# Kernel optimization log

Hardware: AMD Instinct MI355X
Metric: run time of the kernel (lower is better)

## Reference

```python
import jax, jax.numpy as jnp
import numpy as np

LEAKY_SLOPE = 0.2  # tf.nn.leaky_relu default alpha
NEG_INF = -1e9


def setup_inputs() -> dict:
    key = jax.random.key(0)
    k1, k2, k3, k4 = jax.random.split(key, 4)
    B, N, F, D, H = 1, 4096, 128, 64, 4
    features = jax.random.normal(k1, (B, N, F), dtype=jnp.float32)
    adj = jax.random.randint(k2, (N, N), 0, 2, dtype=jnp.int32)  # 0/1 adjacency
    W = jax.random.normal(k3, (H, F, D), dtype=jnp.float32) * 0.1
    attn_k = jax.random.normal(k4, (H, 2 * D, 1), dtype=jnp.float32) * 0.1
    return {"adj": adj, "features": features, "W": W, "attn_k": attn_k}


def reference(adj, features, W, attn_k):
    H, _, D = W.shape
    adj_f = adj.astype(jnp.float32)[None]       # [1, N, N], broadcast over batch
    mask = adj_f != 0.0
    outs = []
    for i in range(H):  # fixed small head loop (heads are structurally distinct weights)
        h = features @ W[i]                      # [B, N, D]
        a_self = h @ attn_k[i, :D]               # [B, N, 1]
        a_neigh = h @ attn_k[i, D:]              # [B, N, 1]
        scores = a_self + jnp.swapaxes(a_neigh, 1, 2)  # [B, N, N] additive scores
        scores = jax.nn.leaky_relu(scores, LEAKY_SLOPE)
        scores = jnp.where(mask, scores, NEG_INF)
        attn = jax.nn.softmax(scores, axis=-1)   # [B, N, N]
        outs.append((attn * adj_f) @ h)          # [B, N, D]
    out = jnp.concatenate(outs, axis=-1) if H > 1 else outs[0]
    return jax.nn.relu(out)
```

## Files before the change

### kernel.cpp

```cpp
#include <hip/hip_runtime.h>
#include <math.h>

#define NN 4096
#define FF 128
#define DD 64
#define HH 4
#define NC 256

typedef _Float16 f16x8 __attribute__((ext_vector_type(8)));
typedef _Float16 f16x2 __attribute__((ext_vector_type(2)));
typedef float    f32x4 __attribute__((ext_vector_type(4)));

__global__ __launch_bounds__(256) void adjbits_kernel(
    const int* __restrict__ adj, unsigned int* __restrict__ adjw)
{
    const int w = blockIdx.x * 256 + threadIdx.x;
    const int4* __restrict__ p = (const int4*)(adj + (size_t)w * 32);
    unsigned int m = 0;
    #pragma unroll
    for (int i = 0; i < 8; ++i) {
        const int4 v = p[i];
        m |= (v.x != 0 ? 1u : 0u) << (i * 4);
        m |= (v.y != 0 ? 2u : 0u) << (i * 4);
        m |= (v.z != 0 ? 4u : 0u) << (i * 4);
        m |= (v.w != 0 ? 8u : 0u) << (i * 4);
    }
    adjw[w] = m;
}

__global__ __launch_bounds__(256) void prep_kernel(
    const float* __restrict__ feats, const float* __restrict__ W,
    const float* __restrict__ ak, _Float16* __restrict__ Bpack,
    _Float16* __restrict__ Es, _Float16* __restrict__ Fs,
    _Float16* __restrict__ En, _Float16* __restrict__ Fn)
{
    __shared__ float Wt[64 * 132];
    __shared__ float ft[32 * 128];
    __shared__ float hlds[32 * 65];
    const int t  = threadIdx.x;
    const int h  = blockIdx.y;
    const int n0 = blockIdx.x * 32;

    {
        const float* Wh = W + h * (FF * DD);
        #pragma unroll
        for (int j = 0; j < 8; ++j) {
            int idx = j * 256 + t;
            int f   = idx >> 4;
            int d4  = idx & 15;
            float4 v = ((const float4*)Wh)[idx];
            Wt[(d4 * 4 + 0) * 132 + f] = v.x;
            Wt[(d4 * 4 + 1) * 132 + f] = v.y;
            Wt[(d4 * 4 + 2) * 132 + f] = v.z;
            Wt[(d4 * 4 + 3) * 132 + f] = v.w;
        }
        #pragma unroll
        for (int j = 0; j < 4; ++j) {
            int idx = j * 256 + t;
            int r = idx >> 5, f4 = idx & 31;
            ((float4*)ft)[r * 32 + f4] = ((const float4*)feats)[(size_t)(n0 + r) * 32 + f4];
        }
    }
    __syncthreads();

    const int d   = t & 63;
    const int wid = t >> 6;
    float acc[8];
    #pragma unroll
    for (int j = 0; j < 8; ++j) acc[j] = 0.f;

    for (int f4 = 0; f4 < 32; ++f4) {
        const float4 w4 = *(const float4*)&Wt[d * 132 + f4 * 4];
        #pragma unroll
        for (int j = 0; j < 8; ++j) {
            const int r = wid + 4 * j;
            const float4 fv = *(const float4*)&ft[r * 128 + f4 * 4];
            acc[j] += fv.x * w4.x + fv.y * w4.y + fv.z * w4.z + fv.w * w4.w;
        }
    }

    const float aks = ak[h * 128 + d];
    const float akn = ak[h * 128 + 64 + d];
    #pragma unroll
    for (int j = 0; j < 8; ++j) {
        const int r = wid + 4 * j;
        const float hv = acc[j];
        hlds[r * 65 + d] = hv;
        float v1 = hv * aks;
        float v2 = hv * akn;
        #pragma unroll
        for (int m = 32; m >= 1; m >>= 1) {
            v1 += __shfl_xor(v1, m, 64);
            v2 += __shfl_xor(v2, m, 64);
        }
        if (d == 0) {
            Es[h * NN + n0 + r] = (_Float16)__expf(v1);
            Fs[h * NN + n0 + r] = (_Float16)__expf(0.2f * v1);
            En[h * NN + n0 + r] = (_Float16)__expf(v2);
            Fn[h * NN + n0 + r] = (_Float16)__expf(0.2f * v2);
        }
    }
    __syncthreads();

    const int cb = t >> 6;
    const int l  = t & 63;
    const int lr = l & 15;
    const int kg = l >> 4;
    f16x8 v;
    #pragma unroll
    for (int j = 0; j < 8; ++j)
        v[j] = (_Float16)hlds[(kg * 8 + j) * 65 + cb * 16 + lr];
    *(f16x8*)(Bpack + ((size_t)(h * 128 + blockIdx.x)) * 2048 + (cb * 64 + l) * 8) = v;
}

__global__ __launch_bounds__(256, 4) void attn_kernel(
    const unsigned int* __restrict__ adjw, const _Float16* __restrict__ Bpack,
    const _Float16* __restrict__ Es, const _Float16* __restrict__ Fs,
    const _Float16* __restrict__ En, const _Float16* __restrict__ Fn,
    float* __restrict__ pacc, float* __restrict__ pden, int ksplit)
{
    __shared__ _Float16 Blds[2][2048];

    const int t  = threadIdx.x;
    const int w  = t >> 6;
    const int l  = t & 63;
    const int lr = l & 15;
    const int kg = l >> 4;
    const int h  = blockIdx.y;
    const int s  = blockIdx.z;
    const int n0 = blockIdx.x * 128 + w * 32;

    const int mstart = s * ksplit;
    const int nchunk = ksplit >> 5;
    const int ncq    = nchunk >> 2;
    const int coff   = blockIdx.x & (ncq - 1);
    const int wb     = mstart >> 5;

#define PC(c) (((((c) >> 2) + coff) & (ncq - 1)) * 4 + ((c) & 3))

    const _Float16 es0 = Es[h * NN + n0 + lr],      fs0 = Fs[h * NN + n0 + lr];
    const _Float16 es1 = Es[h * NN + n0 + 16 + lr], fs1 = Fs[h * NN + n0 + 16 + lr];
    const f16x2 es20 = {es0, es0}, fs20 = {fs0, fs0};
    const f16x2 es21 = {es1, es1}, fs21 = {fs1, fs1};

    const _Float16* __restrict__ EnB = En + (size_t)h * NN;
    const _Float16* __restrict__ FnB = Fn + (size_t)h * NN;
    const int row0 = n0 + lr, row1 = n0 + 16 + lr;

    const _Float16* __restrict__ bp =
        Bpack + ((size_t)(h * 128) + wb) * 2048 + t * 8;

    f32x4 acc[2][4] = {};
    f32x4 dacc[2]   = {};
    f16x8 ones;
    #pragma unroll
    for (int j = 0; j < 8; ++j) ones[j] = (_Float16)1.0f;

    union U8 { f16x8 v; unsigned int u[4]; };

    uint4 sreg = *(const uint4*)(bp + (size_t)PC(0) * 2048);
    *(uint4*)&Blds[0][t * 8] = sreg;
    sreg = *(const uint4*)(bp + (size_t)PC(1) * 2048);
    uint4 enqc = *(const uint4*)(EnB + mstart + PC(0) * 32 + kg * 8);
    uint4 fnqc = *(const uint4*)(FnB + mstart + PC(0) * 32 + kg * 8);
    __syncthreads();

    for (int cq = 0; cq < ncq; ++cq) {
        const int cqp = (cq + coff) & (ncq - 1);
        const uint4 mk0 = *(const uint4*)&adjw[(size_t)row0 * 128 + wb + cqp * 4];
        const uint4 mk1 = *(const uint4*)&adjw[(size_t)row1 * 128 + wb + cqp * 4];

        #pragma unroll
        for (int ci = 0; ci < 4; ++ci) {
            const int c = cq * 4 + ci;

            uint4 nreg;
            {
                const int cn = (c + 2 < nchunk) ? c + 2 : c;
                nreg = *(const uint4*)(bp + (size_t)PC(cn) * 2048);
            }
            if (c + 1 < nchunk)
                *(uint4*)&Blds[(c + 1) & 1][t * 8] = sreg;
            uint4 enq_n, fnq_n;
            {
                const int cn = (c + 1 < nchunk) ? c + 1 : c;
                enq_n = *(const uint4*)(EnB + mstart + PC(cn) * 32 + kg * 8);
                fnq_n = *(const uint4*)(FnB + mstart + PC(cn) * 32 + kg * 8);
            }

            const unsigned int b0 =
                (ci == 0 ? mk0.x : ci == 1 ? mk0.y : ci == 2 ? mk0.z : mk0.w) >> (kg * 8);
            const unsigned int b1 =
                (ci == 0 ? mk1.x : ci == 1 ? mk1.y : ci == 2 ? mk1.z : mk1.w) >> (kg * 8);
            U8 A0, A1;
            #pragma unroll
            for (int p = 0; p < 4; ++p) {
                const unsigned int eu = p == 0 ? enqc.x : p == 1 ? enqc.y : p == 2 ? enqc.z : enqc.w;
                const unsigned int fu = p == 0 ? fnqc.x : p == 1 ? fnqc.y : p == 2 ? fnqc.z : fnqc.w;
                const f16x2 en2 = __builtin_bit_cast(f16x2, eu);
                const f16x2 fn2 = __builtin_bit_cast(f16x2, fu);
                const f16x2 v0 = __builtin_elementwise_max(es20 * en2, fs20 * fn2);
                const f16x2 v1 = __builtin_elementwise_max(es21 * en2, fs21 * fn2);
                const unsigned int mm0 = (((b0 >> (2 * p)) & 1u) ? 0x0000FFFFu : 0u)
                                       | (((b0 >> (2 * p + 1)) & 1u) ? 0xFFFF0000u : 0u);
                const unsigned int mm1 = (((b1 >> (2 * p)) & 1u) ? 0x0000FFFFu : 0u)
                                       | (((b1 >> (2 * p + 1)) & 1u) ? 0xFFFF0000u : 0u);
                A0.u[p] = __builtin_bit_cast(unsigned int, v0) & mm0;
                A1.u[p] = __builtin_bit_cast(unsigned int, v1) & mm1;
            }

            __builtin_amdgcn_s_setprio(1);
            #pragma unroll
            for (int cb = 0; cb < 4; ++cb) {
                const f16x8 Bf = *(const f16x8*)&Blds[c & 1][(cb * 64 + l) * 8];
                acc[0][cb] = __builtin_amdgcn_mfma_f32_16x16x32_f16(A0.v, Bf, acc[0][cb], 0, 0, 0);
                acc[1][cb] = __builtin_amdgcn_mfma_f32_16x16x32_f16(A1.v, Bf, acc[1][cb], 0, 0, 0);
            }
            dacc[0] = __builtin_amdgcn_mfma_f32_16x16x32_f16(A0.v, ones, dacc[0], 0, 0, 0);
            dacc[1] = __builtin_amdgcn_mfma_f32_16x16x32_f16(A1.v, ones, dacc[1], 0, 0, 0);
            __builtin_amdgcn_s_setprio(0);

            __syncthreads();
            sreg = nreg;
            enqc = enq_n;
            fnqc = fnq_n;
        }
    }
#undef PC

    #pragma unroll
    for (int rb = 0; rb < 2; ++rb) {
        #pragma unroll
        for (int r = 0; r < 4; ++r) {
            const int row = n0 + rb * 16 + kg * 4 + r;
            #pragma unroll
            for (int cb = 0; cb < 4; ++cb)
                pacc[((size_t)(s * NN + row)) * NC + h * 64 + cb * 16 + lr] = acc[rb][cb][r];
            if (lr == 0)
                pden[(s * NN + row) * 4 + h] = dacc[rb][r];
        }
    }
}

__global__ __launch_bounds__(256) void finalize_kernel(
    const float* __restrict__ pacc, const float* __restrict__ pden,
    float* __restrict__ out, int nsplit)
{
    const int t = threadIdx.x;
    const int n = blockIdx.x * 4 + (t >> 6);
    const int q = t & 63;
    const int h = q >> 4;

    f32x4 a = {0.f, 0.f, 0.f, 0.f};
    float d = 0.f;
    for (int s = 0; s < nsplit; ++s) {
        a += *(const f32x4*)&pacc[((size_t)(s * NN + n)) * NC + q * 4];
        d += pden[(s * NN + n) * 4 + h];
    }
    f32x4 o;
    const float inv = (d > 0.f) ? 1.0f / d : 0.f;
    #pragma unroll
    for (int i = 0; i < 4; ++i) {
        const float v = a[i] * inv;
        o[i] = v > 0.f ? v : 0.f;
    }
    *(f32x4*)&out[(size_t)n * NC + q * 4] = o;
}

extern "C" void kernel_launch(void* const* d_in, const int* in_sizes, int n_in,
                              void* d_out, int out_size, void* d_ws, size_t ws_size,
                              hipStream_t stream)
{
    const int*   adj   = (const int*)d_in[0];
    const float* feats = (const float*)d_in[1];
    const float* W     = (const float*)d_in[2];
    const float* ak    = (const float*)d_in[3];
    float*       out   = (float*)d_out;

    char* ws = (char*)d_ws;
    unsigned int* adjw  = (unsigned int*)ws;
    _Float16*     Bpack = (_Float16*)(ws + (2ull << 20));
    _Float16*     Es    = (_Float16*)(ws + (4ull << 20));
    _Float16*     Fs    = (_Float16*)(ws + (4ull << 20) + (1 << 16));
    _Float16*     En    = (_Float16*)(ws + (4ull << 20) + (2 << 16));
    _Float16*     Fn    = (_Float16*)(ws + (4ull << 20) + (3 << 16));
    float*        pden  = (float*)(ws + (4ull << 20) + (4 << 16));
    float*        pacc  = (float*)(ws + (5ull << 20));

    int nsplit = 8;
    while (nsplit > 1 && ws_size < (5ull << 20) + (size_t)nsplit * (4ull << 20))
        nsplit >>= 1;
    const int ksplit = NN / nsplit;

    adjbits_kernel<<<2048, 256, 0, stream>>>(adj, adjw);
    prep_kernel<<<dim3(128, 4), 256, 0, stream>>>(feats, W, ak, Bpack, Es, Fs, En, Fn);
    attn_kernel<<<dim3(32, 4, nsplit), 256, 0, stream>>>(adjw, Bpack, Es, Fs, En, Fn,
                                                         pacc, pden, ksplit);
    finalize_kernel<<<1024, 256, 0, stream>>>(pacc, pden, out, nsplit);
}
```

Measured before the change: 55.81 us.

## Pack adjacency bits with wave ballots and use fp16 dot2 in projection

The adjacency bitpacking kernel now has each wave read contiguous int4 rows and build masks with __ballot, which gives fully coalesced loads of the 64MB adjacency matrix. The result is a new interleaved bit layout that the attention kernel decodes with different shift logic. The prep projection now stores W and features in LDS as fp16 and accumulates with fdot2 instead of fp32 FMAs. This lowers projection precision to fp16 inputs, which risks extra error in h and in the attention logits.

```diff
diff --git a/kernel.cpp b/kernel.cpp
--- a/kernel.cpp
+++ b/kernel.cpp
@@ -8,24 +8,31 @@
 #define NC 256
 
 typedef _Float16 f16x8 __attribute__((ext_vector_type(8)));
+typedef _Float16 f16x4 __attribute__((ext_vector_type(4)));
 typedef _Float16 f16x2 __attribute__((ext_vector_type(2)));
 typedef float    f32x4 __attribute__((ext_vector_type(4)));
 
 __global__ __launch_bounds__(256) void adjbits_kernel(
-    const int* __restrict__ adj, unsigned int* __restrict__ adjw)
-{
-    const int w = blockIdx.x * 256 + threadIdx.x;
-    const int4* __restrict__ p = (const int4*)(adj + (size_t)w * 32);
-    unsigned int m = 0;
+    const int* __restrict__ adj, uint4* __restrict__ adjp)
+{
+    const int wid  = blockIdx.x * 4 + (threadIdx.x >> 6);
+    const int lane = threadIdx.x & 63;
+    const int4* __restrict__ base = (const int4*)adj;
     #pragma unroll
     for (int i = 0; i < 8; ++i) {
-        const int4 v = p[i];
-        m |= (v.x != 0 ? 1u : 0u) << (i * 4);
-        m |= (v.y != 0 ? 2u : 0u) << (i * 4);
-        m |= (v.z != 0 ? 4u : 0u) << (i * 4);
-        m |= (v.w != 0 ? 8u : 0u) << (i * 4);
-    }
-    adjw[w] = m;
+        const int g = wid * 8 + i;
+        const int4 v = base[(size_t)g * 64 + lane];
+        unsigned long long b0 = __ballot(v.x != 0);
+        unsigned long long b1 = __ballot(v.y != 0);
+        unsigned long long b2 = __ballot(v.z != 0);
+        unsigned long long b3 = __ballot(v.w != 0);
+        if (lane == 0) {
+            adjp[g * 2] = (uint4){(unsigned)b0, (unsigned)b1,
+                                  (unsigned)b2, (unsigned)b3};
+            adjp[g * 2 + 1] = (uint4){(unsigned)(b0 >> 32), (unsigned)(b1 >> 32),
+                                      (unsigned)(b2 >> 32), (unsigned)(b3 >> 32)};
+        }
+    }
 }
 
 __global__ __launch_bounds__(256) void prep_kernel(
@@ -34,9 +41,9 @@
     _Float16* __restrict__ Es, _Float16* __restrict__ Fs,
     _Float16* __restrict__ En, _Float16* __restrict__ Fn)
 {
-    __shared__ float Wt[64 * 132];
-    __shared__ float ft[32 * 128];
-    __shared__ float hlds[32 * 65];
+    __shared__ _Float16 Wth[64 * 136];
+    __shared__ _Float16 fth[32 * 128];
+    __shared__ float    hlds[32 * 65];
     const int t  = threadIdx.x;
     const int h  = blockIdx.y;
     const int n0 = blockIdx.x * 32;
@@ -49,16 +56,18 @@
             int f   = idx >> 4;
             int d4  = idx & 15;
             float4 v = ((const float4*)Wh)[idx];
-            Wt[(d4 * 4 + 0) * 132 + f] = v.x;
-            Wt[(d4 * 4 + 1) * 132 + f] = v.y;
-            Wt[(d4 * 4 + 2) * 132 + f] = v.z;
-            Wt[(d4 * 4 + 3) * 132 + f] = v.w;
+            Wth[(d4 * 4 + 0) * 136 + f] = (_Float16)v.x;
+            Wth[(d4 * 4 + 1) * 136 + f] = (_Float16)v.y;
+            Wth[(d4 * 4 + 2) * 136 + f] = (_Float16)v.z;
+            Wth[(d4 * 4 + 3) * 136 + f] = (_Float16)v.w;
         }
         #pragma unroll
         for (int j = 0; j < 4; ++j) {
             int idx = j * 256 + t;
             int r = idx >> 5, f4 = idx & 31;
-            ((float4*)ft)[r * 32 + f4] = ((const float4*)feats)[(size_t)(n0 + r) * 32 + f4];
+            float4 v = ((const float4*)feats)[(size_t)(n0 + r) * 32 + f4];
+            f16x4 hv = {(_Float16)v.x, (_Float16)v.y, (_Float16)v.z, (_Float16)v.w};
+            *(f16x4*)&fth[r * 128 + f4 * 4] = hv;
         }
     }
     __syncthreads();
@@ -69,13 +78,20 @@
     #pragma unroll
     for (int j = 0; j < 8; ++j) acc[j] = 0.f;
 
-    for (int f4 = 0; f4 < 32; ++f4) {
-        const float4 w4 = *(const float4*)&Wt[d * 132 + f4 * 4];
+    for (int f8 = 0; f8 < 16; ++f8) {
+        const f16x8 w8 = *(const f16x8*)&Wth[d * 136 + f8 * 8];
+        const f16x2 w0 = __builtin_shufflevector(w8, w8, 0, 1);
+        const f16x2 w1 = __builtin_shufflevector(w8, w8, 2, 3);
+        const f16x2 w2 = __builtin_shufflevector(w8, w8, 4, 5);
+        const f16x2 w3 = __builtin_shufflevector(w8, w8, 6, 7);
         #pragma unroll
         for (int j = 0; j < 8; ++j) {
             const int r = wid + 4 * j;
-            const float4 fv = *(const float4*)&ft[r * 128 + f4 * 4];
-            acc[j] += fv.x * w4.x + fv.y * w4.y + fv.z * w4.z + fv.w * w4.w;
+            const f16x8 fv = *(const f16x8*)&fth[r * 128 + f8 * 8];
+            acc[j] = __builtin_amdgcn_fdot2(w0, __builtin_shufflevector(fv, fv, 0, 1), acc[j], false);
+            acc[j] = __builtin_amdgcn_fdot2(w1, __builtin_shufflevector(fv, fv, 2, 3), acc[j], false);
+            acc[j] = __builtin_amdgcn_fdot2(w2, __builtin_shufflevector(fv, fv, 4, 5), acc[j], false);
+            acc[j] = __builtin_amdgcn_fdot2(w3, __builtin_shufflevector(fv, fv, 6, 7), acc[j], false);
         }
     }
 
@@ -114,7 +130,7 @@
 }
 
 __global__ __launch_bounds__(256, 4) void attn_kernel(
-    const unsigned int* __restrict__ adjw, const _Float16* __restrict__ Bpack,
+    const uint4* __restrict__ adjp, const _Float16* __restrict__ Bpack,
     const _Float16* __restrict__ Es, const _Float16* __restrict__ Fs,
     const _Float16* __restrict__ En, const _Float16* __restrict__ Fn,
     float* __restrict__ pacc, float* __restrict__ pden, int ksplit)
@@ -134,7 +150,7 @@
     const int nchunk = ksplit >> 5;
     const int ncq    = nchunk >> 2;
     const int coff   = blockIdx.x & (ncq - 1);
-    const int wb     = mstart >> 5;
+    const int wqb    = mstart >> 7;
 
 #define PC(c) (((((c) >> 2) + coff) & (ncq - 1)) * 4 + ((c) & 3))
 
@@ -145,10 +161,11 @@
 
     const _Float16* __restrict__ EnB = En + (size_t)h * NN;
     const _Float16* __restrict__ FnB = Fn + (size_t)h * NN;
-    const int row0 = n0 + lr, row1 = n0 + 16 + lr;
+    const uint4* __restrict__ adjpR0 = adjp + (size_t)(n0 + lr) * 32;
+    const uint4* __restrict__ adjpR1 = adjp + (size_t)(n0 + 16 + lr) * 32;
 
     const _Float16* __restrict__ bp =
-        Bpack + ((size_t)(h * 128) + wb) * 2048 + t * 8;
+        Bpack + ((size_t)(h * 128) + (mstart >> 5)) * 2048 + t * 8;
 
     f32x4 acc[2][4] = {};
     f32x4 dacc[2]   = {};
@@ -167,8 +184,8 @@
 
     for (int cq = 0; cq < ncq; ++cq) {
         const int cqp = (cq + coff) & (ncq - 1);
-        const uint4 mk0 = *(const uint4*)&adjw[(size_t)row0 * 128 + wb + cqp * 4];
-        const uint4 mk1 = *(const uint4*)&adjw[(size_t)row1 * 128 + wb + cqp * 4];
+        const uint4 mk0 = adjpR0[wqb + cqp];
+        const uint4 mk1 = adjpR1[wqb + cqp];
 
         #pragma unroll
         for (int ci = 0; ci < 4; ++ci) {
@@ -188,10 +205,21 @@
                 fnq_n = *(const uint4*)(FnB + mstart + PC(cn) * 32 + kg * 8);
             }
 
-            const unsigned int b0 =
-                (ci == 0 ? mk0.x : ci == 1 ? mk0.y : ci == 2 ? mk0.z : mk0.w) >> (kg * 8);
-            const unsigned int b1 =
-                (ci == 0 ? mk1.x : ci == 1 ? mk1.y : ci == 2 ? mk1.z : mk1.w) >> (kg * 8);
+            const int q = ci * 8 + kg * 2;
+            const unsigned int t0 = mk0.x >> q, t1 = mk0.y >> q;
+            const unsigned int t2 = mk0.z >> q, t3 = mk0.w >> q;
+            const unsigned int u0 = mk1.x >> q, u1 = mk1.y >> q;
+            const unsigned int u2 = mk1.z >> q, u3 = mk1.w >> q;
+            unsigned int mmA[4], mmB[4];
+            mmA[0] = ((t0 & 1u) ? 0x0000FFFFu : 0u) | ((t1 & 1u) ? 0xFFFF0000u : 0u);
+            mmA[1] = ((t2 & 1u) ? 0x0000FFFFu : 0u) | ((t3 & 1u) ? 0xFFFF0000u : 0u);
+            mmA[2] = (((t0 >> 1) & 1u) ? 0x0000FFFFu : 0u) | (((t1 >> 1) & 1u) ? 0xFFFF0000u : 0u);
+            mmA[3] = (((t2 >> 1) & 1u) ? 0x0000FFFFu : 0u) | (((t3 >> 1) & 1u) ? 0xFFFF0000u : 0u);
+            mmB[0] = ((u0 & 1u) ? 0x0000FFFFu : 0u) | ((u1 & 1u) ? 0xFFFF0000u : 0u);
+            mmB[1] = ((u2 & 1u) ? 0x0000FFFFu : 0u) | ((u3 & 1u) ? 0xFFFF0000u : 0u);
+            mmB[2] = (((u0 >> 1) & 1u) ? 0x0000FFFFu : 0u) | (((u1 >> 1) & 1u) ? 0xFFFF0000u : 0u);
+            mmB[3] = (((u2 >> 1) & 1u) ? 0x0000FFFFu : 0u) | (((u3 >> 1) & 1u) ? 0xFFFF0000u : 0u);
+
             U8 A0, A1;
             #pragma unroll
             for (int p = 0; p < 4; ++p) {
@@ -201,12 +229,8 @@
                 const f16x2 fn2 = __builtin_bit_cast(f16x2, fu);
                 const f16x2 v0 = __builtin_elementwise_max(es20 * en2, fs20 * fn2);
                 const f16x2 v1 = __builtin_elementwise_max(es21 * en2, fs21 * fn2);
-                const unsigned int mm0 = (((b0 >> (2 * p)) & 1u) ? 0x0000FFFFu : 0u)
-                                       | (((b0 >> (2 * p + 1)) & 1u) ? 0xFFFF0000u : 0u);
-                const unsigned int mm1 = (((b1 >> (2 * p)) & 1u) ? 0x0000FFFFu : 0u)
-                                       | (((b1 >> (2 * p + 1)) & 1u) ? 0xFFFF0000u : 0u);
-                A0.u[p] = __builtin_bit_cast(unsigned int, v0) & mm0;
-                A1.u[p] = __builtin_bit_cast(unsigned int, v1) & mm1;
+                A0.u[p] = __builtin_bit_cast(unsigned int, v0) & mmA[p];
+                A1.u[p] = __builtin_bit_cast(unsigned int, v1) & mmB[p];
             }
 
             __builtin_amdgcn_s_setprio(1);
@@ -278,7 +302,7 @@
     float*       out   = (float*)d_out;
 
     char* ws = (char*)d_ws;
-    unsigned int* adjw  = (unsigned int*)ws;
+    uint4*        adjp  = (uint4*)ws;
     _Float16*     Bpack = (_Float16*)(ws + (2ull << 20));
     _Float16*     Es    = (_Float16*)(ws + (4ull << 20));
     _Float16*     Fs    = (_Float16*)(ws + (4ull << 20) + (1 << 16));
@@ -292,9 +316,9 @@
         nsplit >>= 1;
     const int ksplit = NN / nsplit;
 
-    adjbits_kernel<<<2048, 256, 0, stream>>>(adj, adjw);
+    adjbits_kernel<<<2048, 256, 0, stream>>>(adj, adjp);
     prep_kernel<<<dim3(128, 4), 256, 0, stream>>>(feats, W, ak, Bpack, Es, Fs, En, Fn);
-    attn_kernel<<<dim3(32, 4, nsplit), 256, 0, stream>>>(adjw, Bpack, Es, Fs, En, Fn,
+    attn_kernel<<<dim3(32, 4, nsplit), 256, 0, stream>>>(adjp, Bpack, Es, Fs, En, Fn,
                                                          pacc, pden, ksplit);
     finalize_kernel<<<1024, 256, 0, stream>>>(pacc, pden, out, nsplit);
 }
```

Result: slower. 60.64 us (+8.7%).
